# Performance work log

Hardware: AMD Instinct MI355X
Metric: run time of the kernel (lower is better)

Reference implementation:

```python
import jax, jax.numpy as jnp
import numpy as np

D_MODEL = 1024
N_HEADS = 16
HEAD_DIM = D_MODEL // N_HEADS


def setup_inputs() -> dict:
    key = jax.random.key(0)
    ks = jax.random.split(key, 5)
    x = jax.random.normal(ks[0], (4, 2048, D_MODEL), dtype=jnp.float32)
    # qkv Linear: weight [3*d_model, d_model], bias [3*d_model]
    w_qkv = jax.random.normal(ks[1], (3 * D_MODEL, D_MODEL), dtype=jnp.float32) / np.sqrt(D_MODEL)
    b_qkv = jnp.zeros((3 * D_MODEL,), dtype=jnp.float32)
    w_out = jax.random.normal(ks[2], (D_MODEL, D_MODEL), dtype=jnp.float32) / np.sqrt(D_MODEL)
    b_out = jnp.zeros((D_MODEL,), dtype=jnp.float32)
    return {"x": x, "w_qkv": w_qkv, "b_qkv": b_qkv, "w_out": w_out, "b_out": b_out}


def reference(x, w_qkv, b_qkv, w_out, b_out):
    B, T, C = x.shape
    H, Dh = N_HEADS, HEAD_DIM
    qkv = x @ w_qkv.T + b_qkv                      # [B,T,3C]
    qkv = qkv.reshape(B, T, 3, H, Dh)
    q = jnp.transpose(qkv[:, :, 0], (0, 2, 1, 3))  # [B,H,T,Dh]
    k = jnp.transpose(qkv[:, :, 1], (0, 2, 1, 3))
    v = jnpp_transpose = jnp.transpose(qkv[:, :, 2], (0, 2, 1, 3))
    scale = 1.0 / np.sqrt(Dh).astype(np.float32)
    att = jnp.einsum('bhqd,bhkd->bhqk', q, k) * scale
    causal = jnp.tril(jnp.ones((T, T), dtype=bool))
    att = jnp.where(causal[None, None], att, -jnp.inf)
    att = jax.nn.softmax(att, axis=-1)
    head_out = jnp.einsum('bhqk,bhkd->bhqd', att, v)  # [B,H,T,Dh]
    out = jnp.transpose(head_out, (0, 2, 1, 3)).reshape(B, T, C)
    return out @ w_out.T + b_out
```

## Files before the change

### kernel.cpp

```cpp
#include <hip/hip_runtime.h>
#include <hip/hip_bf16.h>


#define D_MODEL 1024
#define N_HEADS 16
#define HEAD_DIM 64
#define SEQ 2048
#define BATCH 4

typedef __attribute__((ext_vector_type(8))) short bf16x8;
typedef __attribute__((ext_vector_type(4))) float f32x4;
typedef unsigned int uint;

__device__ __forceinline__ short f2bf(float f) {
    union { float f; uint i; } c; c.f = f;
    uint x = c.i;
    x += 0x7fffu + ((x >> 16) & 1u);
    return (short)(x >> 16);
}
__device__ __forceinline__ uint pack2(float a, float b) {
    return (uint)(unsigned short)f2bf(a) | ((uint)(unsigned short)f2bf(b) << 16);
}
__device__ __forceinline__ uint asu(float f) { union { float f; uint i; } c; c.f = f; return c.i; }
__device__ __forceinline__ uint packtr(float lo, float hi) {
    return __builtin_amdgcn_perm(asu(hi), asu(lo), 0x07060302u);
}

__device__ __forceinline__ void glds16(const void* g, void* l) {
    __builtin_amdgcn_global_load_lds(
        (const __attribute__((address_space(1))) uint*)g,
        (__attribute__((address_space(3))) uint*)l, 16, 0, 0);
}

__global__ __launch_bounds__(256) void cvt3_bf16(const float* __restrict__ s0,
                                                 const float* __restrict__ s1,
                                                 const float* __restrict__ s2,
                                                 short* __restrict__ dst,
                                                 int n0, int n01) {
    int i = blockIdx.x * 256 + threadIdx.x;
    const float* src;
    int off;
    if (i < n0)       { src = s0; off = i; }
    else if (i < n01) { src = s1; off = i - n0; }
    else              { src = s2; off = i - n01; }
    float4 f = *(const float4*)(src + (size_t)off * 4);
    uint2 o; o.x = pack2(f.x, f.y); o.y = pack2(f.z, f.w);
    *(uint2*)(dst + (size_t)i * 4) = o;
}

template <int MODE>
__global__ __launch_bounds__(256, 2) void gemm_bt(
    const short* __restrict__ A, const short* __restrict__ B,
    const float* __restrict__ bias, float* __restrict__ Cp,
    int M, int N, int K,
    short* __restrict__ qp, short* __restrict__ kp, short* __restrict__ vp)
{
    __shared__ short As[2][128][32];
    __shared__ short Bs[2][128][32];
    const int tid = threadIdx.x;
    const int wave = tid >> 6, lane = tid & 63;
    const int quad = lane >> 4, l16 = lane & 15;
    const int wm = (wave >> 1) * 64, wn = (wave & 1) * 64;
    const int rowBase = blockIdx.y * 128;
    const int colBase = blockIdx.x * 128;

    const short* gA = A + (size_t)(rowBase + wave * 32 + (lane >> 2)) * K + (lane & 3) * 8;
    const short* gB = B + (size_t)(colBase + wave * 32 + (lane >> 2)) * K + (lane & 3) * 8;

    f32x4 acc[4][4] = {};
    const int NT = K / 32;

#define GSTAGE(buf, k0)                                                \
    {                                                                  \
        glds16(gA + (k0), &As[buf][wave * 32][0]);                     \
        glds16(gA + (size_t)16 * K + (k0), &As[buf][wave * 32 + 16][0]); \
        glds16(gB + (k0), &Bs[buf][wave * 32][0]);                     \
        glds16(gB + (size_t)16 * K + (k0), &Bs[buf][wave * 32 + 16][0]); \
    }

    GSTAGE(0, 0)
    __syncthreads();

    for (int t = 0; t < NT; ++t) {
        const int cur = t & 1;
        if (t + 1 < NT) GSTAGE(cur ^ 1, (t + 1) * 32)
        bf16x8 af[4], bfr[4];
#pragma unroll
        for (int i = 0; i < 4; ++i)
            af[i] = *(const bf16x8*)&As[cur][wm + i * 16 + l16][quad * 8];
#pragma unroll
        for (int j = 0; j < 4; ++j)
            bfr[j] = *(const bf16x8*)&Bs[cur][wn + j * 16 + l16][quad * 8];
#pragma unroll
        for (int i = 0; i < 4; ++i)
#pragma unroll
            for (int j = 0; j < 4; ++j)
                acc[i][j] = __builtin_amdgcn_mfma_f32_16x16x32_bf16(af[i], bfr[j], acc[i][j], 0, 0, 0);
        __syncthreads();
    }
#undef GSTAGE

#pragma unroll
    for (int i = 0; i < 4; ++i) {
#pragma unroll
        for (int j = 0; j < 4; ++j) {
#pragma unroll
            for (int r = 0; r < 4; ++r) {
                int row = rowBase + wm + i * 16 + quad * 4 + r;
                int col = colBase + wn + j * 16 + l16;
                float v = acc[i][j][r] + bias[col];
                if (MODE == 0) {
                    Cp[(size_t)row * N + col] = v;
                } else {
                    int which = col >> 10;
                    int h = (col >> 6) & 15;
                    int d = col & 63;
                    int b = row >> 11;
                    int t2 = row & 2047;
                    short* dst = (which == 0) ? qp : (which == 1) ? kp : vp;
                    dst[((((size_t)b * N_HEADS + h) * SEQ) + t2) * HEAD_DIM + d] = f2bf(v);
                }
            }
        }
    }
}

__global__ __launch_bounds__(256, 2) void attn_fwd(
    const short* __restrict__ Q, const short* __restrict__ K,
    const short* __restrict__ V, short* __restrict__ O)
{
    __shared__ short Ks[2][64][72];
    __shared__ short Vt[2][64][72];
    __shared__ short Ps[128][72];
    const int tid = threadIdx.x;
    const int wave = tid >> 6, lane = tid & 63;
    const int quad = lane >> 4, l16 = lane & 15;
    const int bh = blockIdx.x;
    const int b = bh >> 4, h = bh & 15;
    const int qt = gridDim.y - 1 - blockIdx.y;
    const int qbase = qt * 128;
    const short* Qh = Q + (size_t)bh * SEQ * HEAD_DIM;
    const short* Kh = K + (size_t)bh * SEQ * HEAD_DIM;
    const short* Vh = V + (size_t)bh * SEQ * HEAD_DIM;

    const float C1 = 0.125f * 1.44269504f;
    const float C2 = 14.4269504f;

    bf16x8 onesf;
#pragma unroll
    for (int e = 0; e < 8; ++e) onesf[e] = (short)0x3F80;

    bf16x8 qf[2][2];
#pragma unroll
    for (int m = 0; m < 2; ++m)
#pragma unroll
        for (int st = 0; st < 2; ++st)
            qf[m][st] = *(const bf16x8*)(Qh + (size_t)(qbase + wave * 32 + m * 16 + l16) * HEAD_DIM + st * 32 + quad * 8);

    f32x4 o[2][4] = {};
    f32x4 osum[2] = {};

    const int subw = qbase + wave * 32;
    const int subS = __builtin_amdgcn_readfirstlane(subw);

    const int kr = tid >> 2, kc = (tid & 3) * 16;
    const int vk = (tid & 31) * 2, vd = (tid >> 5) * 8;

    const int ntiles = 2 * qt + 2;
    int4 kv0 = *(const int4*)(Kh + (size_t)kr * HEAD_DIM + kc);
    int4 kv1 = *(const int4*)(Kh + (size_t)kr * HEAD_DIM + kc + 8);
    int4 vv0 = *(const int4*)(Vh + (size_t)vk * HEAD_DIM + vd);
    int4 vv1 = *(const int4*)(Vh + (size_t)(vk + 1) * HEAD_DIM + vd);

    for (int j = 0; j < ntiles; ++j) {
        const int kb = j * 64;
        const int p = j & 1;
        *(int4*)&Ks[p][kr][kc] = kv0;
        *(int4*)&Ks[p][kr][kc + 8] = kv1;
        {
            const uint* pa = (const uint*)&vv0;
            const uint* pb = (const uint*)&vv1;
#pragma unroll
            for (int e = 0; e < 4; ++e) {
                uint lo = __builtin_amdgcn_perm(pb[e], pa[e], 0x05040100u);
                uint hi = __builtin_amdgcn_perm(pb[e], pa[e], 0x07060302u);
                *(uint*)&Vt[p][vd + 2 * e][vk] = lo;
                *(uint*)&Vt[p][vd + 2 * e + 1][vk] = hi;
            }
        }
        if (j + 1 < ntiles) {
            const int kbn = kb + 64;
            kv0 = *(const int4*)(Kh + (size_t)(kbn + kr) * HEAD_DIM + kc);
            kv1 = *(const int4*)(Kh + (size_t)(kbn + kr) * HEAD_DIM + kc + 8);
            vv0 = *(const int4*)(Vh + (size_t)(kbn + vk) * HEAD_DIM + vd);
            vv1 = *(const int4*)(Vh + (size_t)(kbn + vk + 1) * HEAD_DIM + vd);
        }
        __syncthreads();

        if (kb > subS + 31) continue;

        {
            const int prowb = wave * 32 + l16;
#pragma unroll
            for (int kt = 0; kt < 4; ++kt) {
                const int kbkt = kb + kt * 16;
                bf16x8 kf0, kf1;
                if (kbkt <= subS + 31) {
                    kf0 = *(const bf16x8*)&Ks[p][kt * 16 + l16][quad * 8];
                    kf1 = *(const bf16x8*)&Ks[p][kt * 16 + l16][32 + quad * 8];
                }
#pragma unroll
                for (int m = 0; m < 2; ++m) {
                    const int sub = subS + m * 16;
                    uint2 u;
                    if (kbkt > sub + 15) {
                        u.x = 0u; u.y = 0u;
                    } else {
                        f32x4 tt = {0.f, 0.f, 0.f, 0.f};
                        tt = __builtin_amdgcn_mfma_f32_16x16x32_bf16(kf0, qf[m][0], tt, 0, 0, 0);
                        tt = __builtin_amdgcn_mfma_f32_16x16x32_bf16(kf1, qf[m][1], tt, 0, 0, 0);
                        float pp[4];
                        if (kbkt + 15 <= sub) {
#pragma unroll
                            for (int r = 0; r < 4; ++r)
                                pp[r] = __builtin_exp2f(__builtin_fmaf(tt[r], C1, -C2));
                        } else {
                            const int qrow = sub + l16;
#pragma unroll
                            for (int r = 0; r < 4; ++r) {
                                float a = __builtin_fmaf(tt[r], C1, -C2);
                                if (kbkt + quad * 4 + r > qrow) a = -1e30f;
                                pp[r] = __builtin_exp2f(a);
                            }
                        }
                        u.x = packtr(pp[0], pp[1]); u.y = packtr(pp[2], pp[3]);
                    }
                    *(uint2*)&Ps[prowb + m * 16][kt * 16 + quad * 4] = u;
                }
            }
        }
#pragma unroll
        for (int st = 0; st < 2; ++st) {
            if (st == 1 && kb + 32 > subS + 31) break;
            bf16x8 pf0 = *(const bf16x8*)&Ps[wave * 32 + l16][st * 32 + quad * 8];
            bf16x8 pf1 = *(const bf16x8*)&Ps[wave * 32 + 16 + l16][st * 32 + quad * 8];
            __builtin_amdgcn_s_setprio(1);
            osum[0] = __builtin_amdgcn_mfma_f32_16x16x32_bf16(pf0, onesf, osum[0], 0, 0, 0);
            osum[1] = __builtin_amdgcn_mfma_f32_16x16x32_bf16(pf1, onesf, osum[1], 0, 0, 0);
#pragma unroll
            for (int dt = 0; dt < 4; ++dt) {
                bf16x8 vf = *(const bf16x8*)&Vt[p][dt * 16 + l16][st * 32 + quad * 8];
                o[0][dt] = __builtin_amdgcn_mfma_f32_16x16x32_bf16(pf0, vf, o[0][dt], 0, 0, 0);
                o[1][dt] = __builtin_amdgcn_mfma_f32_16x16x32_bf16(pf1, vf, o[1][dt], 0, 0, 0);
            }
            __builtin_amdgcn_s_setprio(0);
        }
    }

#pragma unroll
    for (int m = 0; m < 2; ++m) {
#pragma unroll
        for (int r = 0; r < 4; ++r) {
            float inv = 1.f / osum[m][r];
            int t = qbase + wave * 32 + m * 16 + quad * 4 + r;
            size_t base = ((size_t)b * SEQ + t) * D_MODEL + h * HEAD_DIM;
#pragma unroll
            for (int dt = 0; dt < 4; ++dt)
                O[base + dt * 16 + l16] = f2bf(o[m][dt][r] * inv);
        }
    }
}

extern "C" void kernel_launch(void* const* d_in, const int* in_sizes, int n_in,
                              void* d_out, int out_size, void* d_ws, size_t ws_size,
                              hipStream_t stream)
{
    const float* x     = (const float*)d_in[0];
    const float* w_qkv = (const float*)d_in[1];
    const float* b_qkv = (const float*)d_in[2];
    const float* w_out = (const float*)d_in[3];
    const float* b_out = (const float*)d_in[4];
    float* out = (float*)d_out;

    const int NX = BATCH * SEQ * D_MODEL;
    const int NWQ = 3 * D_MODEL * D_MODEL;
    const int NWO = D_MODEL * D_MODEL;
    const size_t HE = (size_t)BATCH * N_HEADS * SEQ * HEAD_DIM;

    short* xb    = (short*)d_ws;
    short* wqkvb = xb + NX;
    short* woutb = wqkvb + NWQ;
    short* qp    = woutb + NWO;
    short* kp    = qp + HE;
    short* vp    = kp + HE;
    short* ho    = xb;

    const int M = BATCH * SEQ;

    cvt3_bf16<<<(NX + NWQ + NWO) / 1024, 256, 0, stream>>>(
        x, w_qkv, w_out, xb, NX / 4, (NX + NWQ) / 4);

    gemm_bt<1><<<dim3(3 * D_MODEL / 128, M / 128), 256, 0, stream>>>(
        xb, wqkvb, b_qkv, nullptr, M, 3 * D_MODEL, D_MODEL, qp, kp, vp);

    attn_fwd<<<dim3(BATCH * N_HEADS, SEQ / 128), 256, 0, stream>>>(qp, kp, vp, ho);

    gemm_bt<0><<<dim3(D_MODEL / 128, M / 128), 256, 0, stream>>>(
        ho, woutb, b_out, out, M, D_MODEL, D_MODEL, nullptr, nullptr, nullptr);
}
```

Before: 261.4 us.

## Single-buffer K/V tiles and interleave causal query-tile order across blocks

Drops the double-buffered K and V shared-memory tiles in favour of single buffers guarded by two barriers per iteration, which shrinks LDS use and could allow more resident blocks. It also remaps blockIdx.y to query tiles in a zig-zag order (15..12, 8..11, 7..4, 0..3) so heavy and light causal tiles are mixed for better load balance. The cost is an extra __syncthreads per K tile and less overlap between LDS writes and compute.

```diff
diff --git a/kernel.cpp b/kernel.cpp
--- a/kernel.cpp
+++ b/kernel.cpp
@@ -129,15 +129,16 @@
     const short* __restrict__ Q, const short* __restrict__ K,
     const short* __restrict__ V, short* __restrict__ O)
 {
-    __shared__ short Ks[2][64][72];
-    __shared__ short Vt[2][64][72];
+    __shared__ short Ks[64][72];
+    __shared__ short Vt[64][72];
     __shared__ short Ps[128][72];
     const int tid = threadIdx.x;
     const int wave = tid >> 6, lane = tid & 63;
     const int quad = lane >> 4, l16 = lane & 15;
     const int bh = blockIdx.x;
     const int b = bh >> 4, h = bh & 15;
-    const int qt = gridDim.y - 1 - blockIdx.y;
+    const int y = blockIdx.y, y0 = y & 3, g = y >> 2;
+    const int qt = (g == 0) ? 15 - y0 : (g == 1) ? 8 + y0 : (g == 2) ? 7 - y0 : y0;
     const int qbase = qt * 128;
     const short* Qh = Q + (size_t)bh * SEQ * HEAD_DIM;
     const short* Kh = K + (size_t)bh * SEQ * HEAD_DIM;
@@ -174,9 +175,9 @@
 
     for (int j = 0; j < ntiles; ++j) {
         const int kb = j * 64;
-        const int p = j & 1;
-        *(int4*)&Ks[p][kr][kc] = kv0;
-        *(int4*)&Ks[p][kr][kc + 8] = kv1;
+        __syncthreads();
+        *(int4*)&Ks[kr][kc] = kv0;
+        *(int4*)&Ks[kr][kc + 8] = kv1;
         {
             const uint* pa = (const uint*)&vv0;
             const uint* pb = (const uint*)&vv1;
@@ -184,10 +185,12 @@
             for (int e = 0; e < 4; ++e) {
                 uint lo = __builtin_amdgcn_perm(pb[e], pa[e], 0x05040100u);
                 uint hi = __builtin_amdgcn_perm(pb[e], pa[e], 0x07060302u);
-                *(uint*)&Vt[p][vd + 2 * e][vk] = lo;
-                *(uint*)&Vt[p][vd + 2 * e + 1][vk] = hi;
+                *(uint*)&Vt[vd + 2 * e][vk] = lo;
+                *(uint*)&Vt[vd + 2 * e + 1][vk] = hi;
             }
         }
+        __syncthreads();
+
         if (j + 1 < ntiles) {
             const int kbn = kb + 64;
             kv0 = *(const int4*)(Kh + (size_t)(kbn + kr) * HEAD_DIM + kc);
@@ -195,7 +198,6 @@
             vv0 = *(const int4*)(Vh + (size_t)(kbn + vk) * HEAD_DIM + vd);
             vv1 = *(const int4*)(Vh + (size_t)(kbn + vk + 1) * HEAD_DIM + vd);
         }
-        __syncthreads();
 
         if (kb > subS + 31) continue;
 
@@ -206,8 +208,8 @@
                 const int kbkt = kb + kt * 16;
                 bf16x8 kf0, kf1;
                 if (kbkt <= subS + 31) {
-                    kf0 = *(const bf16x8*)&Ks[p][kt * 16 + l16][quad * 8];
-                    kf1 = *(const bf16x8*)&Ks[p][kt * 16 + l16][32 + quad * 8];
+                    kf0 = *(const bf16x8*)&Ks[kt * 16 + l16][quad * 8];
+                    kf1 = *(const bf16x8*)&Ks[kt * 16 + l16][32 + quad * 8];
                 }
 #pragma unroll
                 for (int m = 0; m < 2; ++m) {
@@ -219,21 +221,21 @@
                         f32x4 tt = {0.f, 0.f, 0.f, 0.f};
                         tt = __builtin_amdgcn_mfma_f32_16x16x32_bf16(kf0, qf[m][0], tt, 0, 0, 0);
                         tt = __builtin_amdgcn_mfma_f32_16x16x32_bf16(kf1, qf[m][1], tt, 0, 0, 0);
-                        float pp[4];
+                        float p[4];
                         if (kbkt + 15 <= sub) {
 #pragma unroll
                             for (int r = 0; r < 4; ++r)
-                                pp[r] = __builtin_exp2f(__builtin_fmaf(tt[r], C1, -C2));
+                                p[r] = __builtin_exp2f(__builtin_fmaf(tt[r], C1, -C2));
                         } else {
                             const int qrow = sub + l16;
 #pragma unroll
                             for (int r = 0; r < 4; ++r) {
                                 float a = __builtin_fmaf(tt[r], C1, -C2);
                                 if (kbkt + quad * 4 + r > qrow) a = -1e30f;
-                                pp[r] = __builtin_exp2f(a);
+                                p[r] = __builtin_exp2f(a);
                             }
                         }
-                        u.x = packtr(pp[0], pp[1]); u.y = packtr(pp[2], pp[3]);
+                        u.x = packtr(p[0], p[1]); u.y = packtr(p[2], p[3]);
                     }
                     *(uint2*)&Ps[prowb + m * 16][kt * 16 + quad * 4] = u;
                 }
@@ -249,7 +251,7 @@
             osum[1] = __builtin_amdgcn_mfma_f32_16x16x32_bf16(pf1, onesf, osum[1], 0, 0, 0);
 #pragma unroll
             for (int dt = 0; dt < 4; ++dt) {
-                bf16x8 vf = *(const bf16x8*)&Vt[p][dt * 16 + l16][st * 32 + quad * 8];
+                bf16x8 vf = *(const bf16x8*)&Vt[dt * 16 + l16][st * 32 + quad * 8];
                 o[0][dt] = __builtin_amdgcn_mfma_f32_16x16x32_bf16(pf0, vf, o[0][dt], 0, 0, 0);
                 o[1][dt] = __builtin_amdgcn_mfma_f32_16x16x32_bf16(pf1, vf, o[1][dt], 0, 0, 0);
             }
```

Result: faster. 252.9 us (-3.3%).
